# Optimization experiments

Measured on AMD Instinct MI355X. Metric: run time of the kernel, lower is better.

The kernel has to match this reference:

```python
import jax, jax.numpy as jnp
import numpy as np

HEADS = 8
DIM_HEAD = 40
QUERY_DIM = 320          # == inner_dim = HEADS * DIM_HEAD
CONTEXT_DIM = 768
INNER = HEADS * DIM_HEAD


def setup_inputs() -> dict:
    key = jax.random.key(0)
    ks = jax.random.split(key, 8)
    B, NQ, NK = 32, 4096, 77
    s_q = 1.0 / np.sqrt(QUERY_DIM)
    s_c = 1.0 / np.sqrt(CONTEXT_DIM)
    s_i = 1.0 / np.sqrt(INNER)
    return {
        "x": jax.random.normal(ks[0], (B, NQ, QUERY_DIM), jnp.float32),
        "context": jax.random.normal(ks[1], (B, NK, CONTEXT_DIM), jnp.float32),
        "Wq": jax.random.normal(ks[2], (INNER, QUERY_DIM), jnp.float32) * s_q,
        "Wk": jax.random.normal(ks[3], (INNER, CONTEXT_DIM), jnp.float32) * s_c,
        "Wv": jax.random.normal(ks[4], (INNER, CONTEXT_DIM), jnp.float32) * s_c,
        "Wo": jax.random.normal(ks[5], (QUERY_DIM, INNER), jnp.float32) * s_i,
        "bo": jnp.zeros((QUERY_DIM,), jnp.float32),
        "gamma_q": jnp.ones((INNER,), jnp.float32),
        "gamma_k": jnp.ones((INNER,), jnp.float32),
        "gamma_v": jnp.ones((INNER,), jnp.float32),
        "gamma_out": jnp.ones((INNER,), jnp.float32),
    }


def reference(x, context, Wq, Wk, Wv, Wo, bo, gamma_q, gamma_k, gamma_v, gamma_out):
    B, NQ, _ = x.shape
    NK = context.shape[1]
    # linear projections (bias=False) followed by per-channel gamma scaling
    q = (x @ Wq.T) * gamma_q            # [B, NQ, INNER]
    k = (context @ Wk.T) * gamma_k      # [B, NK, INNER]
    v = (context @ Wv.T) * gamma_v      # [B, NK, INNER]
    # split heads: b n (h d) -> b h n d
    q = q.reshape(B, NQ, HEADS, DIM_HEAD).transpose(0, 2, 1, 3)
    k = k.reshape(B, NK, HEADS, DIM_HEAD).transpose(0, 2, 1, 3)
    v = v.reshape(B, NK, HEADS, DIM_HEAD).transpose(0, 2, 1, 3)
    scale = DIM_HEAD ** -0.5
    scores = jnp.einsum("bhqd,bhkd->bhqk", q, k) * scale  # [B,H,NQ,NK]
    attn = jax.nn.softmax(scores, axis=-1)
    o = jnp.einsum("bhqk,bhkd->bhqd", attn, v)            # [B,H,NQ,Dh]
    o = o.transpose(0, 2, 1, 3).reshape(B, NQ, INNER)
    # output projection (with bias) then gamma_out scale; dropout p=0 -> identity
    return (o @ Wo.T + bo) * gamma_out
```

## Files before the change

kernel.cpp:

```cpp
#include <hip/hip_runtime.h>

#define B_   32
#define NQ_  4096
#define NK_  77
#define H_   8
#define DH_  40
#define IN_  320
#define CD_  768
#define M_   (B_ * NQ_)
#define MKV_ (B_ * NK_)

#define NKP_  80
#define NKP2_ 96
#define DHP_  48
#define KQ_   64

typedef __attribute__((ext_vector_type(8))) short bf16x8;
typedef __attribute__((ext_vector_type(4))) float f32x4;
typedef unsigned short ushort_t;

__device__ __forceinline__ unsigned short f2bf(float f) {
  union { float f; unsigned int i; } v; v.f = f;
  unsigned int i = v.i;
  i += 0x7fffu + ((i >> 16) & 1u);
  return (unsigned short)(i >> 16);
}
__device__ __forceinline__ unsigned int pack2(float a, float b) {
  return (unsigned int)f2bf(a) | ((unsigned int)f2bf(b) << 16);
}

__global__ __launch_bounds__(256) void wcvt(
    const float* __restrict__ Wq, const float* __restrict__ Wo,
    const float* __restrict__ Wk, const float* __restrict__ Wv,
    unsigned short* __restrict__ Wqb, unsigned short* __restrict__ Wob,
    unsigned short* __restrict__ Wkb, unsigned short* __restrict__ Wvb)
{
  const int i = blockIdx.x * 256 + threadIdx.x;
  const float* src;
  unsigned short* dst;
  int n;
  switch (blockIdx.y) {
    case 0:  src = Wq; dst = Wqb; n = IN_ * IN_ / 4; break;
    case 1:  src = Wo; dst = Wob; n = IN_ * IN_ / 4; break;
    case 2:  src = Wk; dst = Wkb; n = IN_ * CD_ / 4; break;
    default: src = Wv; dst = Wvb; n = IN_ * CD_ / 4; break;
  }
  if (i >= n) return;
  const float4 v = ((const float4*)src)[i];
  uint2 p; p.x = pack2(v.x, v.y); p.y = pack2(v.z, v.w);
  ((uint2*)dst)[i] = p;
}

__global__ __launch_bounds__(256) void kv_mfma(
    const float* __restrict__ ctx, const unsigned short* __restrict__ Wkb,
    const unsigned short* __restrict__ Wvb, const float* __restrict__ gk,
    const float* __restrict__ gv, unsigned short* __restrict__ Khb,
    unsigned short* __restrict__ Vtb)
{
  constexpr int LDA = 40;
  __shared__ alignas(16) unsigned short As[64 * LDA];
  __shared__ alignas(16) unsigned short Bs[64 * LDA];
  const int m0 = blockIdx.x * 64;
  const int n0 = blockIdx.y * 64;
  const int isV = blockIdx.z;
  const unsigned short* Wb = isV ? Wvb : Wkb;
  const int tid = threadIdx.x;
  const int wave = tid >> 6;
  const int lane = tid & 63;
  const int lm = lane & 15;
  const int quad = lane >> 4;

  f32x4 acc0 = {0.f, 0.f, 0.f, 0.f};
  f32x4 acc1 = acc0, acc2 = acc0, acc3 = acc0;

  for (int k0 = 0; k0 < CD_; k0 += 32) {
#pragma unroll
    for (int c = tid; c < 512; c += 256) {
      const int row = c >> 3, kq = (c & 7) << 2;
      const int fr = m0 + row;
      float4 v = {0.f, 0.f, 0.f, 0.f};
      if (fr < MKV_)
        v = *(const float4*)(ctx + (size_t)fr * CD_ + k0 + kq);
      uint2 p; p.x = pack2(v.x, v.y); p.y = pack2(v.z, v.w);
      *(uint2*)(&As[row * LDA + kq]) = p;
    }
    {
      const int row = tid >> 2, kq = (tid & 3) << 3;
      *(uint4*)(&Bs[row * LDA + kq]) =
          *(const uint4*)(Wb + (size_t)(n0 + row) * CD_ + k0 + kq);
    }
    __syncthreads();
    const bf16x8 a  = *(const bf16x8*)(&As[(wave * 16 + lm) * LDA + quad * 8]);
    const bf16x8 b0 = *(const bf16x8*)(&Bs[( 0 + lm) * LDA + quad * 8]);
    const bf16x8 b1 = *(const bf16x8*)(&Bs[(16 + lm) * LDA + quad * 8]);
    const bf16x8 b2 = *(const bf16x8*)(&Bs[(32 + lm) * LDA + quad * 8]);
    const bf16x8 b3 = *(const bf16x8*)(&Bs[(48 + lm) * LDA + quad * 8]);
    acc0 = __builtin_amdgcn_mfma_f32_16x16x32_bf16(a, b0, acc0, 0, 0, 0);
    acc1 = __builtin_amdgcn_mfma_f32_16x16x32_bf16(a, b1, acc1, 0, 0, 0);
    acc2 = __builtin_amdgcn_mfma_f32_16x16x32_bf16(a, b2, acc2, 0, 0, 0);
    acc3 = __builtin_amdgcn_mfma_f32_16x16x32_bf16(a, b3, acc3, 0, 0, 0);
    __syncthreads();
  }

  const float* g = isV ? gv : gk;
  const f32x4 accs[4] = {acc0, acc1, acc2, acc3};
#pragma unroll
  for (int t = 0; t < 4; ++t) {
    const int col = n0 + t * 16 + lm;
    const int h = col / DH_, d = col % DH_;
    const float gc = g[col];
#pragma unroll
    for (int r = 0; r < 4; ++r) {
      const int row = m0 + wave * 16 + quad * 4 + r;
      if (row < MKV_) {
        const int bb = row / NK_, pos = row % NK_;
        const unsigned short val = f2bf(accs[t][r] * gc);
        if (!isV)
          Khb[((size_t)(bb * H_ + h) * NKP_ + pos) * KQ_ + d] = val;
        else
          Vtb[((size_t)(bb * H_ + h) * DHP_ + d) * NKP2_ + pos] = val;
      }
    }
  }
}

template <int MODE>
__global__ __launch_bounds__(256) void gemm_strip(
    const void* __restrict__ Ap, const unsigned short* __restrict__ Wb,
    const float* __restrict__ gamma, const float* __restrict__ bias,
    void* __restrict__ Cp)
{
  constexpr int LDB = 328;
  __shared__ alignas(16) unsigned short Bs[64 * LDB];
  const int m0 = blockIdx.x * 64;
  const int tid = threadIdx.x;
  const int wave = tid >> 6;
  const int lane = tid & 63;
  const int lm = lane & 15;
  const int quad = lane >> 4;
  const int arow = m0 + wave * 16 + lm;

  bf16x8 a[10];
  if (MODE == 0) {
    const float* A = (const float*)Ap;
#pragma unroll
    for (int kf = 0; kf < 10; ++kf) {
      const float* p = A + (size_t)arow * IN_ + kf * 32 + quad * 8;
      const float4 v0 = *(const float4*)(p);
      const float4 v1 = *(const float4*)(p + 4);
      union { uint4 u; bf16x8 h; } cv;
      cv.u.x = pack2(v0.x, v0.y); cv.u.y = pack2(v0.z, v0.w);
      cv.u.z = pack2(v1.x, v1.y); cv.u.w = pack2(v1.z, v1.w);
      a[kf] = cv.h;
    }
  } else {
    const unsigned short* A = (const unsigned short*)Ap;
#pragma unroll
    for (int kf = 0; kf < 10; ++kf)
      a[kf] = *(const bf16x8*)(A + (size_t)arow * IN_ + kf * 32 + quad * 8);
  }

  const int srow = tid >> 2;
  const int sc0 = tid & 3;

  for (int nc = 0; nc < 5; ++nc) {
    if (nc) __syncthreads();
    {
      const unsigned short* src = Wb + (size_t)(nc * 64 + srow) * IN_;
      unsigned short* dst = &Bs[srow * LDB];
#pragma unroll
      for (int j = 0; j < 10; ++j) {
        const int c = (sc0 + j * 4) * 8;
        *(uint4*)(dst + c) = *(const uint4*)(src + c);
      }
    }
    __syncthreads();

    f32x4 acc[4];
#pragma unroll
    for (int nf = 0; nf < 4; ++nf) acc[nf] = (f32x4){0.f, 0.f, 0.f, 0.f};
#pragma unroll
    for (int kf = 0; kf < 10; ++kf) {
#pragma unroll
      for (int nf = 0; nf < 4; ++nf) {
        const bf16x8 b =
            *(const bf16x8*)(&Bs[(nf * 16 + lm) * LDB + kf * 32 + quad * 8]);
        acc[nf] = __builtin_amdgcn_mfma_f32_16x16x32_bf16(a[kf], b, acc[nf], 0, 0, 0);
      }
    }

#pragma unroll
    for (int nf = 0; nf < 4; ++nf) {
      const int col = nc * 64 + nf * 16 + lm;
      const float g = gamma[col];
      if (MODE == 0) {
#pragma unroll
        for (int r = 0; r < 4; ++r) {
          const int row = m0 + wave * 16 + quad * 4 + r;
          ((unsigned short*)Cp)[(size_t)row * IN_ + col] = f2bf(acc[nf][r] * g);
        }
      } else {
        const float bb = bias[col];
#pragma unroll
        for (int r = 0; r < 4; ++r) {
          const int row = m0 + wave * 16 + quad * 4 + r;
          ((float*)Cp)[(size_t)row * IN_ + col] = (acc[nf][r] + bb) * g;
        }
      }
    }
  }
}

#define QT_ 128
__global__ __launch_bounds__(256) void attn_mfma(
    const unsigned short* __restrict__ Khb,
    const unsigned short* __restrict__ Vtb,
    unsigned short* __restrict__ QO)
{
  __shared__ alignas(16) unsigned short smem[14976 + 48 * 104];
  unsigned short* Qs = smem;
  unsigned short* Ks = smem + 128 * 72;
  unsigned short* Vt = smem + 14976;
  unsigned short* Ps = smem;

  const int b = blockIdx.z, h = blockIdx.y, qt = blockIdx.x;
  const int tid = threadIdx.x;
  const int row0 = qt * QT_;
  const size_t qbase = ((size_t)b * NQ_ + row0) * IN_ + h * DH_;

  for (int i = tid; i < QT_ * 9; i += 256) {
    const int row = i / 9, seg = i % 9;
    uint4 v = {0u, 0u, 0u, 0u};
    if (seg < 5)
      v = *(const uint4*)(QO + qbase + (size_t)row * IN_ + seg * 8);
    *(uint4*)(&Qs[row * 72 + seg * 8]) = v;
  }
  {
    const unsigned short* src = Khb + (size_t)(b * H_ + h) * NKP_ * KQ_;
    for (int i = tid; i < NKP_ * 9; i += 256) {
      const int row = i / 9, seg = i % 9;
      uint4 v = {0u, 0u, 0u, 0u};
      if (seg < 8) v = *(const uint4*)(src + row * KQ_ + seg * 8);
      *(uint4*)(&Ks[row * 72 + seg * 8]) = v;
    }
  }
  {
    const unsigned short* src = Vtb + (size_t)(b * H_ + h) * DHP_ * NKP2_;
    for (int i = tid; i < DHP_ * 12; i += 256) {
      const int row = i / 12, seg = i % 12;
      *(uint4*)(&Vt[row * 104 + seg * 8]) =
          *(const uint4*)(src + row * NKP2_ + seg * 8);
    }
  }
  __syncthreads();

  const int wave = tid >> 6;
  const int lane = tid & 63;
  const int lm = lane & 15;
  const int quad = lane >> 4;
  const int wrow = wave * 32;

  f32x4 sacc[2][5];
#pragma unroll
  for (int mf = 0; mf < 2; ++mf)
#pragma unroll
    for (int t = 0; t < 5; ++t) sacc[mf][t] = (f32x4){0.f, 0.f, 0.f, 0.f};

#pragma unroll
  for (int k = 0; k < 2; ++k) {
    bf16x8 aq[2];
#pragma unroll
    for (int mf = 0; mf < 2; ++mf)
      aq[mf] = *(const bf16x8*)(&Qs[(wrow + mf * 16 + lm) * 72 + k * 32 + quad * 8]);
#pragma unroll
    for (int t = 0; t < 5; ++t) {
      const bf16x8 bk = *(const bf16x8*)(&Ks[(t * 16 + lm) * 72 + k * 32 + quad * 8]);
#pragma unroll
      for (int mf = 0; mf < 2; ++mf)
        sacc[mf][t] = __builtin_amdgcn_mfma_f32_16x16x32_bf16(aq[mf], bk, sacc[mf][t], 0, 0, 0);
    }
  }

  const float scale = 0.15811388300841897f;
  float sv[2][5][4];
  float rl[2][4];
#pragma unroll
  for (int mf = 0; mf < 2; ++mf) {
#pragma unroll
    for (int t = 0; t < 5; ++t)
#pragma unroll
      for (int r = 0; r < 4; ++r) {
        float v = sacc[mf][t][r] * scale;
        if (t == 4 && lm >= 13) v = -1e30f;
        sv[mf][t][r] = v;
      }
#pragma unroll
    for (int r = 0; r < 4; ++r) {
      float m = sv[mf][0][r];
#pragma unroll
      for (int t = 1; t < 5; ++t) m = fmaxf(m, sv[mf][t][r]);
#pragma unroll
      for (int d = 1; d < 16; d <<= 1) m = fmaxf(m, __shfl_xor(m, d));
      float l = 0.f;
#pragma unroll
      for (int t = 0; t < 5; ++t) {
        const float e = __expf(sv[mf][t][r] - m);
        sv[mf][t][r] = e;
        l += e;
      }
#pragma unroll
      for (int d = 1; d < 16; d <<= 1) l += __shfl_xor(l, d);
      rl[mf][r] = 1.f / l;
    }
  }

  __syncthreads();

  unsigned short* Pw = Ps + wave * 32 * 104;
#pragma unroll
  for (int mf = 0; mf < 2; ++mf)
#pragma unroll
    for (int t = 0; t < 5; ++t)
#pragma unroll
      for (int r = 0; r < 4; ++r)
        Pw[(mf * 16 + quad * 4 + r) * 104 + t * 16 + lm] = f2bf(sv[mf][t][r]);
  {
    const int row = lane >> 1, half = lane & 1;
    *(uint4*)(&Pw[row * 104 + 80 + half * 8]) = (uint4){0u, 0u, 0u, 0u};
  }
  __syncthreads();

  f32x4 oacc[2][3];
#pragma unroll
  for (int mf = 0; mf < 2; ++mf)
#pragma unroll
    for (int n = 0; n < 3; ++n) oacc[mf][n] = (f32x4){0.f, 0.f, 0.f, 0.f};

#pragma unroll
  for (int k = 0; k < 3; ++k) {
    bf16x8 ap[2];
#pragma unroll
    for (int mf = 0; mf < 2; ++mf)
      ap[mf] = *(const bf16x8*)(&Pw[(mf * 16 + lm) * 104 + k * 32 + quad * 8]);
#pragma unroll
    for (int n = 0; n < 3; ++n) {
      const bf16x8 bv = *(const bf16x8*)(&Vt[(n * 16 + lm) * 104 + k * 32 + quad * 8]);
#pragma unroll
      for (int mf = 0; mf < 2; ++mf)
        oacc[mf][n] = __builtin_amdgcn_mfma_f32_16x16x32_bf16(ap[mf], bv, oacc[mf][n], 0, 0, 0);
    }
  }

#pragma unroll
  for (int mf = 0; mf < 2; ++mf)
#pragma unroll
    for (int n = 0; n < 3; ++n) {
      const int col = n * 16 + lm;
      if (col < DH_) {
#pragma unroll
        for (int r = 0; r < 4; ++r) {
          const int row = wrow + mf * 16 + quad * 4 + r;
          QO[qbase + (size_t)row * IN_ + col] = f2bf(oacc[mf][n][r] * rl[mf][r]);
        }
      }
    }
}

extern "C" void kernel_launch(void* const* d_in, const int* in_sizes, int n_in,
                              void* d_out, int out_size, void* d_ws,
                              size_t ws_size, hipStream_t stream)
{
  const float* x   = (const float*)d_in[0];
  const float* ctx = (const float*)d_in[1];
  const float* Wq  = (const float*)d_in[2];
  const float* Wk  = (const float*)d_in[3];
  const float* Wv  = (const float*)d_in[4];
  const float* Wo  = (const float*)d_in[5];
  const float* bo  = (const float*)d_in[6];
  const float* gq  = (const float*)d_in[7];
  const float* gk  = (const float*)d_in[8];
  const float* gv  = (const float*)d_in[9];
  const float* go  = (const float*)d_in[10];
  float* out = (float*)d_out;

  char* ws = (char*)d_ws;
  unsigned short* q_ws = (unsigned short*)ws;
  size_t off = (size_t)M_ * IN_ * 2;
  unsigned short* Khb = (unsigned short*)(ws + off); off += (size_t)B_ * H_ * NKP_ * KQ_ * 2;
  unsigned short* Vtb = (unsigned short*)(ws + off); off += (size_t)B_ * H_ * DHP_ * NKP2_ * 2;
  unsigned short* Wqb = (unsigned short*)(ws + off); off += (size_t)IN_ * IN_ * 2;
  unsigned short* Wob = (unsigned short*)(ws + off);
  unsigned short* Wkb = (unsigned short*)ws;
  unsigned short* Wvb = (unsigned short*)(ws + (size_t)IN_ * CD_ * 2);

  hipMemsetAsync(Khb, 0, (size_t)B_ * H_ * NKP_ * KQ_ * 2, stream);
  hipMemsetAsync(Vtb, 0, (size_t)B_ * H_ * DHP_ * NKP2_ * 2, stream);

  wcvt<<<dim3(IN_ * CD_ / 4 / 256, 4), dim3(256), 0, stream>>>(
      Wq, Wo, Wk, Wv, Wqb, Wob, Wkb, Wvb);
  kv_mfma<<<dim3((MKV_ + 63) / 64, IN_ / 64, 2), dim3(256), 0, stream>>>(
      ctx, Wkb, Wvb, gk, gv, Khb, Vtb);
  gemm_strip<0><<<dim3(M_ / 64), dim3(256), 0, stream>>>(
      x, Wqb, gq, nullptr, q_ws);
  attn_mfma<<<dim3(NQ_ / QT_, H_, B_), dim3(256), 0, stream>>>(Khb, Vtb, q_ws);
  gemm_strip<1><<<dim3(M_ / 64), dim3(256), 0, stream>>>(
      q_ws, Wob, go, bo, out);
}
```

Measured before the change: 486.7 us.

## Drop LDS weight staging in strip GEMM; load B fragments directly, double rows per wave

```diff
diff --git a/kernel.cpp b/kernel.cpp
--- a/kernel.cpp
+++ b/kernel.cpp
@@ -130,62 +130,65 @@
     const float* __restrict__ gamma, const float* __restrict__ bias,
     void* __restrict__ Cp)
 {
-  constexpr int LDB = 328;
-  __shared__ alignas(16) unsigned short Bs[64 * LDB];
-  const int m0 = blockIdx.x * 64;
+  const int m0 = blockIdx.x * 128;
   const int tid = threadIdx.x;
   const int wave = tid >> 6;
   const int lane = tid & 63;
   const int lm = lane & 15;
   const int quad = lane >> 4;
-  const int arow = m0 + wave * 16 + lm;
-
-  bf16x8 a[10];
+  const int wrow = m0 + wave * 32;
+
+  bf16x8 a[2][10];
   if (MODE == 0) {
     const float* A = (const float*)Ap;
 #pragma unroll
-    for (int kf = 0; kf < 10; ++kf) {
-      const float* p = A + (size_t)arow * IN_ + kf * 32 + quad * 8;
-      const float4 v0 = *(const float4*)(p);
-      const float4 v1 = *(const float4*)(p + 4);
-      union { uint4 u; bf16x8 h; } cv;
-      cv.u.x = pack2(v0.x, v0.y); cv.u.y = pack2(v0.z, v0.w);
-      cv.u.z = pack2(v1.x, v1.y); cv.u.w = pack2(v1.z, v1.w);
-      a[kf] = cv.h;
+    for (int mf = 0; mf < 2; ++mf) {
+      const float* rp = A + (size_t)(wrow + mf * 16 + lm) * IN_ + quad * 8;
+#pragma unroll
+      for (int kf = 0; kf < 10; ++kf) {
+        const float4 v0 = *(const float4*)(rp + kf * 32);
+        const float4 v1 = *(const float4*)(rp + kf * 32 + 4);
+        union { uint4 u; bf16x8 h; } cv;
+        cv.u.x = pack2(v0.x, v0.y); cv.u.y = pack2(v0.z, v0.w);
+        cv.u.z = pack2(v1.x, v1.y); cv.u.w = pack2(v1.z, v1.w);
+        a[mf][kf] = cv.h;
+      }
     }
   } else {
     const unsigned short* A = (const unsigned short*)Ap;
 #pragma unroll
-    for (int kf = 0; kf < 10; ++kf)
-      a[kf] = *(const bf16x8*)(A + (size_t)arow * IN_ + kf * 32 + quad * 8);
-  }
-
-  const int srow = tid >> 2;
-  const int sc0 = tid & 3;
+    for (int mf = 0; mf < 2; ++mf) {
+      const unsigned short* rp = A + (size_t)(wrow + mf * 16 + lm) * IN_ + quad * 8;
+#pragma unroll
+      for (int kf = 0; kf < 10; ++kf)
+        a[mf][kf] = *(const bf16x8*)(rp + kf * 32);
+    }
+  }
+
+  const unsigned short* bb0 = Wb + (size_t)( 0 + lm) * IN_ + quad * 8;
+  const unsigned short* bb1 = Wb + (size_t)(16 + lm) * IN_ + quad * 8;
+  const unsigned short* bb2 = Wb + (size_t)(32 + lm) * IN_ + quad * 8;
+  const unsigned short* bb3 = Wb + (size_t)(48 + lm) * IN_ + quad * 8;
 
   for (int nc = 0; nc < 5; ++nc) {
-    if (nc) __syncthreads();
-    {
-      const unsigned short* src = Wb + (size_t)(nc * 64 + srow) * IN_;
-      unsigned short* dst = &Bs[srow * LDB];
-#pragma unroll
-      for (int j = 0; j < 10; ++j) {
-        const int c = (sc0 + j * 4) * 8;
-        *(uint4*)(dst + c) = *(const uint4*)(src + c);
-      }
-    }
-    __syncthreads();
-
-    f32x4 acc[4];
-#pragma unroll
-    for (int nf = 0; nf < 4; ++nf) acc[nf] = (f32x4){0.f, 0.f, 0.f, 0.f};
+    f32x4 acc[2][4];
+#pragma unroll
+    for (int mf = 0; mf < 2; ++mf)
+#pragma unroll
+      for (int nf = 0; nf < 4; ++nf) acc[mf][nf] = (f32x4){0.f, 0.f, 0.f, 0.f};
+
 #pragma unroll
     for (int kf = 0; kf < 10; ++kf) {
-#pragma unroll
-      for (int nf = 0; nf < 4; ++nf) {
-        const bf16x8 b =
-            *(const bf16x8*)(&Bs[(nf * 16 + lm) * LDB + kf * 32 + quad * 8]);
-        acc[nf] = __builtin_amdgcn_mfma_f32_16x16x32_bf16(a[kf], b, acc[nf], 0, 0, 0);
+      const bf16x8 b0 = *(const bf16x8*)(bb0 + kf * 32);
+      const bf16x8 b1 = *(const bf16x8*)(bb1 + kf * 32);
+      const bf16x8 b2 = *(const bf16x8*)(bb2 + kf * 32);
+      const bf16x8 b3 = *(const bf16x8*)(bb3 + kf * 32);
+#pragma unroll
+      for (int mf = 0; mf < 2; ++mf) {
+        acc[mf][0] = __builtin_amdgcn_mfma_f32_16x16x32_bf16(a[mf][kf], b0, acc[mf][0], 0, 0, 0);
+        acc[mf][1] = __builtin_amdgcn_mfma_f32_16x16x32_bf16(a[mf][kf], b1, acc[mf][1], 0, 0, 0);
+        acc[mf][2] = __builtin_amdgcn_mfma_f32_16x16x32_bf16(a[mf][kf], b2, acc[mf][2], 0, 0, 0);
+        acc[mf][3] = __builtin_amdgcn_mfma_f32_16x16x32_bf16(a[mf][kf], b3, acc[mf][3], 0, 0, 0);
       }
     }
 
@@ -195,19 +198,24 @@
       const float g = gamma[col];
       if (MODE == 0) {
 #pragma unroll
-        for (int r = 0; r < 4; ++r) {
-          const int row = m0 + wave * 16 + quad * 4 + r;
-          ((unsigned short*)Cp)[(size_t)row * IN_ + col] = f2bf(acc[nf][r] * g);
-        }
+        for (int mf = 0; mf < 2; ++mf)
+#pragma unroll
+          for (int r = 0; r < 4; ++r) {
+            const int row = wrow + mf * 16 + quad * 4 + r;
+            ((unsigned short*)Cp)[(size_t)row * IN_ + col] = f2bf(acc[mf][nf][r] * g);
+          }
       } else {
-        const float bb = bias[col];
-#pragma unroll
-        for (int r = 0; r < 4; ++r) {
-          const int row = m0 + wave * 16 + quad * 4 + r;
-          ((float*)Cp)[(size_t)row * IN_ + col] = (acc[nf][r] + bb) * g;
-        }
-      }
-    }
+        const float bbv = bias[col];
+#pragma unroll
+        for (int mf = 0; mf < 2; ++mf)
+#pragma unroll
+          for (int r = 0; r < 4; ++r) {
+            const int row = wrow + mf * 16 + quad * 4 + r;
+            ((float*)Cp)[(size_t)row * IN_ + col] = (acc[mf][nf][r] + bbv) * g;
+          }
+      }
+    }
+    bb0 += 64 * IN_; bb1 += 64 * IN_; bb2 += 64 * IN_; bb3 += 64 * IN_;
   }
 }
 
@@ -400,9 +408,9 @@
       Wq, Wo, Wk, Wv, Wqb, Wob, Wkb, Wvb);
   kv_mfma<<<dim3((MKV_ + 63) / 64, IN_ / 64, 2), dim3(256), 0, stream>>>(
       ctx, Wkb, Wvb, gk, gv, Khb, Vtb);
-  gemm_strip<0><<<dim3(M_ / 64), dim3(256), 0, stream>>>(
+  gemm_strip<0><<<dim3(M_ / 128), dim3(256), 0, stream>>>(
       x, Wqb, gq, nullptr, q_ws);
   attn_mfma<<<dim3(NQ_ / QT_, H_, B_), dim3(256), 0, stream>>>(Khb, Vtb, q_ws);
-  gemm_strip<1><<<dim3(M_ / 64), dim3(256), 0, stream>>>(
+  gemm_strip<1><<<dim3(M_ / 128), dim3(256), 0, stream>>>(
       q_ws, Wob, go, bo, out);
 }
```

Result: slower. 618.0 us (+27.0%).

## Prefetch weight strips into registers and store them in fragment-major LDS layout

Applied to the files above, without the earlier changes.

```diff
diff --git a/kernel.cpp b/kernel.cpp
--- a/kernel.cpp
+++ b/kernel.cpp
@@ -125,13 +125,12 @@
 }
 
 template <int MODE>
-__global__ __launch_bounds__(256) void gemm_strip(
+__global__ __launch_bounds__(256, 4) void gemm_strip(
     const void* __restrict__ Ap, const unsigned short* __restrict__ Wb,
     const float* __restrict__ gamma, const float* __restrict__ bias,
     void* __restrict__ Cp)
 {
-  constexpr int LDB = 328;
-  __shared__ alignas(16) unsigned short Bs[64 * LDB];
+  __shared__ alignas(16) unsigned short Bs[40 * 64 * 8];
   const int m0 = blockIdx.x * 64;
   const int tid = threadIdx.x;
   const int wave = tid >> 6;
@@ -140,14 +139,27 @@
   const int quad = lane >> 4;
   const int arow = m0 + wave * 16 + lm;
 
+  const int sr = tid >> 2;
+  const int sc = tid & 3;
+  const int snf = sr >> 4;
+  const int slm = sr & 15;
+
+  uint4 rB[10];
+  {
+    const unsigned short* src = Wb + (size_t)sr * IN_;
+#pragma unroll
+    for (int j = 0; j < 10; ++j)
+      rB[j] = *(const uint4*)(src + (sc + j * 4) * 8);
+  }
+
   bf16x8 a[10];
   if (MODE == 0) {
     const float* A = (const float*)Ap;
+    const float* rp = A + (size_t)arow * IN_ + quad * 8;
 #pragma unroll
     for (int kf = 0; kf < 10; ++kf) {
-      const float* p = A + (size_t)arow * IN_ + kf * 32 + quad * 8;
-      const float4 v0 = *(const float4*)(p);
-      const float4 v1 = *(const float4*)(p + 4);
+      const float4 v0 = *(const float4*)(rp + kf * 32);
+      const float4 v1 = *(const float4*)(rp + kf * 32 + 4);
       union { uint4 u; bf16x8 h; } cv;
       cv.u.x = pack2(v0.x, v0.y); cv.u.y = pack2(v0.z, v0.w);
       cv.u.z = pack2(v1.x, v1.y); cv.u.w = pack2(v1.z, v1.w);
@@ -155,26 +167,24 @@
     }
   } else {
     const unsigned short* A = (const unsigned short*)Ap;
+    const unsigned short* rp = A + (size_t)arow * IN_ + quad * 8;
 #pragma unroll
     for (int kf = 0; kf < 10; ++kf)
-      a[kf] = *(const bf16x8*)(A + (size_t)arow * IN_ + kf * 32 + quad * 8);
-  }
-
-  const int srow = tid >> 2;
-  const int sc0 = tid & 3;
+      a[kf] = *(const bf16x8*)(rp + kf * 32);
+  }
 
   for (int nc = 0; nc < 5; ++nc) {
     if (nc) __syncthreads();
-    {
-      const unsigned short* src = Wb + (size_t)(nc * 64 + srow) * IN_;
-      unsigned short* dst = &Bs[srow * LDB];
-#pragma unroll
-      for (int j = 0; j < 10; ++j) {
-        const int c = (sc0 + j * 4) * 8;
-        *(uint4*)(dst + c) = *(const uint4*)(src + c);
-      }
-    }
+#pragma unroll
+    for (int j = 0; j < 10; ++j)
+      *(uint4*)(&Bs[(((snf * 10) + j) * 64 + sc * 16 + slm) * 8]) = rB[j];
     __syncthreads();
+    if (nc < 4) {
+      const unsigned short* src = Wb + (size_t)((nc + 1) * 64 + sr) * IN_;
+#pragma unroll
+      for (int j = 0; j < 10; ++j)
+        rB[j] = *(const uint4*)(src + (sc + j * 4) * 8);
+    }
 
     f32x4 acc[4];
 #pragma unroll
@@ -184,7 +194,7 @@
 #pragma unroll
       for (int nf = 0; nf < 4; ++nf) {
         const bf16x8 b =
-            *(const bf16x8*)(&Bs[(nf * 16 + lm) * LDB + kf * 32 + quad * 8]);
+            *(const bf16x8*)(&Bs[((nf * 10 + kf) * 64 + lane) * 8]);
         acc[nf] = __builtin_amdgcn_mfma_f32_16x16x32_bf16(a[kf], b, acc[nf], 0, 0, 0);
       }
     }
@@ -200,11 +210,11 @@
           ((unsigned short*)Cp)[(size_t)row * IN_ + col] = f2bf(acc[nf][r] * g);
         }
       } else {
-        const float bb = bias[col];
+        const float bbv = bias[col];
 #pragma unroll
         for (int r = 0; r < 4; ++r) {
           const int row = m0 + wave * 16 + quad * 4 + r;
-          ((float*)Cp)[(size_t)row * IN_ + col] = (acc[nf][r] + bb) * g;
+          ((float*)Cp)[(size_t)row * IN_ + col] = (acc[nf][r] + bbv) * g;
         }
       }
     }
```

Measured after the change: 756.6 us. 55.4% more time.
